# Kernel tuning notes

Measured on AMD Instinct MI355X. Metric: run time of the kernel, lower is better.

Reference implementation:

```python
import jax, jax.numpy as jnp
import numpy as np

N = 100000      # nodes
E = 1200000     # edges
D_IN = 128      # input_dim
H = 64          # hidden_dim
OUT = 3         # output_dim
EPS = 1e-5      # BatchNorm eps


def setup_inputs() -> dict:
    key = jax.random.key(0)
    ks = jax.random.split(key, 24)
    w = lambda k, shape: jax.random.normal(k, shape, jnp.float32) * 0.05
    return {
        "x": jax.random.normal(ks[0], (N, D_IN), jnp.float32),
        "edge_index": jax.random.randint(ks[1], (2, E), 0, N, dtype=jnp.int32),
        "proj_W": w(ks[2], (H, D_IN)), "proj_b": w(ks[3], (H,)),
        "conv1_W": w(ks[4], (H, H)), "conv1_b": w(ks[5], (H,)),
        "bn1_g": jnp.ones((H,), jnp.float32), "bn1_b": w(ks[6], (H,)),
        "conv2_W": w(ks[7], (H, H)), "conv2_b": w(ks[8], (H,)),
        "bn2_g": jnp.ones((H,), jnp.float32), "bn2_b": w(ks[9], (H,)),
        "conv3_W": w(ks[10], (H, H)), "conv3_b": w(ks[11], (H,)),
        "bn3_g": jnp.ones((H,), jnp.float32), "bn3_b": w(ks[12], (H,)),
        "byp_W": w(ks[13], (OUT, D_IN)), "byp_b": w(ks[14], (OUT,)),
        "head_W": w(ks[15], (OUT, H + OUT)), "head_b": w(ks[16], (OUT,)),
    }


def reference(x, edge_index, proj_W, proj_b,
              conv1_W, conv1_b, bn1_g, bn1_b,
              conv2_W, conv2_b, bn2_g, bn2_b,
              conv3_W, conv3_b, bn3_g, bn3_b,
              byp_W, byp_b, head_W, head_b):
    n = x.shape[0]
    row, col = edge_index[0], edge_index[1]
    loop = jnp.arange(n, dtype=row.dtype)
    row_f = jnp.concatenate([row, loop])   # source (with self loops)
    col_f = jnp.concatenate([col, loop])   # target
    # symmetric GCN normalization: deg over targets of A+I, edge weight 1
    deg = jax.ops.segment_sum(jnp.ones(row_f.shape, jnp.float32), col_f, num_segments=n)
    dinv = jnp.where(deg > 0, jax.lax.rsqrt(deg), 0.0)
    norm = dinv[row_f] * dinv[col_f]       # [E+N]

    def gcn(h, W, b):
        h = h @ W.T                                    # transform then propagate
        msg = h[row_f] * norm[:, None]                 # gather + scale
        return jax.ops.segment_sum(msg, col_f, num_segments=n) + b

    def bn(h, g, b):
        # eval-mode BatchNorm1d: running_mean=0, running_var=1 buffers
        return h * (g / jnp.sqrt(1.0 + EPS)) + b

    h = x @ proj_W.T + proj_b
    idn = h
    h = jax.nn.relu(bn(gcn(h, conv1_W, conv1_b), bn1_g, bn1_b)) + idn  # dropout inactive (eval)
    idn = h
    h = jax.nn.relu(bn(gcn(h, conv2_W, conv2_b), bn2_g, bn2_b)) + idn
    h = jax.nn.relu(bn(gcn(h, conv3_W, conv3_b), bn3_g, bn3_b))

    byp = x @ byp_W.T + byp_b
    p = jnp.concatenate([h, byp], axis=1) @ head_W.T + head_b
    kappa = jnp.clip(p[:, 0] * 5.0 + 2.5, 0.2, 10.0)
    alpha = p[:, 1]
    tau = jnp.clip(p[:, 2] + 0.5, 0.05, 2.0)
    return jnp.stack([kappa, alpha, tau], axis=1)
```

## Files before the change

kernel.cpp:

```cpp
#include <hip/hip_runtime.h>
#include <hip/hip_fp16.h>

#define NN 100000
#define NE 1200000
#define NBUK ((NN + 127) / 128)
#define NCHUNK 128

typedef _Float16 h8 __attribute__((ext_vector_type(8)));
typedef float f32x4 __attribute__((ext_vector_type(4)));

__global__ __launch_bounds__(1024) void k_zerob(int* bcnt) {
    int i = threadIdx.x;
    if (i <= NBUK) bcnt[i] = 0;
}

__global__ __launch_bounds__(256) void k_bhist(const int* __restrict__ col, int* __restrict__ bcnt) {
    __shared__ int lh[NBUK];
    for (int i = threadIdx.x; i < NBUK; i += 256) lh[i] = 0;
    __syncthreads();
    for (int e = blockIdx.x * 256 + threadIdx.x; e < NE; e += 256 * 256)
        atomicAdd(&lh[col[e] >> 7], 1);
    __syncthreads();
    for (int i = threadIdx.x; i < NBUK; i += 256) {
        int v = lh[i];
        if (v) atomicAdd(&bcnt[i], v);
    }
}

__global__ __launch_bounds__(1024) void k_bscan(int* __restrict__ bcnt, int* __restrict__ bcur) {
    __shared__ int s[1024];
    int tid = threadIdx.x;
    int v = (tid < NBUK) ? bcnt[tid] : 0;
    s[tid] = v;
    __syncthreads();
    #pragma unroll
    for (int d = 1; d < 1024; d <<= 1) {
        int t = (tid >= d) ? s[tid - d] : 0;
        __syncthreads();
        s[tid] += t;
        __syncthreads();
    }
    if (tid < NBUK) {
        int excl = s[tid] - v;
        bcnt[tid] = excl;
        bcur[tid] = excl;
    }
    if (tid == 0) bcnt[NBUK] = NE;
}

__global__ __launch_bounds__(256) void k_bucket(const int* __restrict__ row,
                                                const int* __restrict__ col,
                                                int* __restrict__ bcur,
                                                unsigned* __restrict__ tmp) {
    __shared__ int lh[NBUK];
    const int tid = threadIdx.x;
    const int per = (NE + NCHUNK - 1) / NCHUNK;
    const int e0 = blockIdx.x * per;
    const int e1 = (e0 + per < NE) ? (e0 + per) : NE;
    for (int i = tid; i < NBUK; i += 256) lh[i] = 0;
    __syncthreads();
    for (int e = e0 + tid; e < e1; e += 256)
        atomicAdd(&lh[col[e] >> 7], 1);
    __syncthreads();
    for (int b = tid; b < NBUK; b += 256) {
        int c = lh[b];
        if (c) lh[b] = atomicAdd(&bcur[b], c);
    }
    __syncthreads();
    for (int e = e0 + tid; e < e1; e += 256) {
        int c = col[e], r = row[e];
        int pos = atomicAdd(&lh[c >> 7], 1);
        tmp[pos] = ((unsigned)r << 7) | (unsigned)(c & 127);
    }
}

__global__ __launch_bounds__(256) void k_build(const unsigned* __restrict__ tmp,
                                               const int* __restrict__ bbase,
                                               int* __restrict__ off,
                                               float* __restrict__ dinv,
                                               int* __restrict__ csr_row) {
    __shared__ int cnt[128], s[128], cur[128];
    const int b = blockIdx.x, tid = threadIdx.x;
    const int colBase = b << 7;
    const int nCols = (NN - colBase < 128) ? (NN - colBase) : 128;
    const int seg0 = bbase[b], seg1 = bbase[b + 1];
    if (tid < 128) cnt[tid] = 0;
    __syncthreads();
    for (int i = seg0 + tid; i < seg1; i += 256)
        atomicAdd(&cnt[tmp[i] & 127], 1);
    __syncthreads();
    if (tid < 128) s[tid] = cnt[tid];
    __syncthreads();
    #pragma unroll
    for (int d = 1; d < 128; d <<= 1) {
        int t = (tid < 128 && tid >= d) ? s[tid - d] : 0;
        __syncthreads();
        if (tid < 128) s[tid] += t;
        __syncthreads();
    }
    if (tid < nCols) {
        int exc = seg0 + s[tid] - cnt[tid];
        off[colBase + tid] = exc;
        cur[tid] = exc;
        dinv[colBase + tid] = rsqrtf((float)cnt[tid] + 1.0f);
    }
    if (b == 0 && tid == 0) off[NN] = NE;
    __syncthreads();
    for (int i = seg0 + tid; i < seg1; i += 256) {
        unsigned v = tmp[i];
        int pos = atomicAdd(&cur[v & 127u], 1);
        csr_row[pos] = (int)(v >> 7);
    }
}

__global__ __launch_bounds__(256) void k_gemmP(const float* __restrict__ X,
                                               const float* __restrict__ W,
                                               const float* __restrict__ bias,
                                               _Float16* __restrict__ Yh,
                                               const float* __restrict__ bypW,
                                               const float* __restrict__ bypb,
                                               float* __restrict__ bypOut,
                                               int n_nodes) {
    constexpr int D = 128, RS = D + 8, KS = D / 32;
    __shared__ _Float16 Xh[64 * RS];
    __shared__ _Float16 Wh[64 * RS];
    const int tid = threadIdx.x;
    const int n0 = blockIdx.x * 64;

    for (int i = tid; i < 64 * (D / 8); i += 256) {
        int j = i / (D / 8), d8 = (i % (D / 8)) * 8;
        const float4* wp = (const float4*)&W[j * D + d8];
        float4 w0 = wp[0], w1 = wp[1];
        h8 h = { (_Float16)w0.x, (_Float16)w0.y, (_Float16)w0.z, (_Float16)w0.w,
                 (_Float16)w1.x, (_Float16)w1.y, (_Float16)w1.z, (_Float16)w1.w };
        *(h8*)&Wh[j * RS + d8] = h;
    }
    for (int i = tid; i < 64 * (D / 8); i += 256) {
        int nl = i / (D / 8), d8 = (i % (D / 8)) * 8;
        int n = n0 + nl; if (n >= n_nodes) n = n_nodes - 1;
        const float4* xp = (const float4*)&X[(size_t)n * D + d8];
        float4 x0 = xp[0], x1 = xp[1];
        h8 h = { (_Float16)x0.x, (_Float16)x0.y, (_Float16)x0.z, (_Float16)x0.w,
                 (_Float16)x1.x, (_Float16)x1.y, (_Float16)x1.z, (_Float16)x1.w };
        *(h8*)&Xh[nl * RS + d8] = h;
    }
    __syncthreads();

    const int wid = tid >> 6, lane = tid & 63;
    const int lm = lane & 15, lq = lane >> 4;
    const int mBase = wid * 16;

    h8 bfrag[4][KS];
    #pragma unroll
    for (int t = 0; t < 4; ++t)
        #pragma unroll
        for (int s = 0; s < KS; ++s)
            bfrag[t][s] = *(const h8*)&Wh[(t * 16 + lm) * RS + s * 32 + lq * 8];

    h8 bfragB[KS];
    #pragma unroll
    for (int s = 0; s < KS; ++s) {
        if (lm < 3) {
            const float4* wp = (const float4*)&bypW[lm * D + s * 32 + lq * 8];
            float4 w0 = wp[0], w1 = wp[1];
            bfragB[s] = (h8){ (_Float16)w0.x, (_Float16)w0.y, (_Float16)w0.z, (_Float16)w0.w,
                              (_Float16)w1.x, (_Float16)w1.y, (_Float16)w1.z, (_Float16)w1.w };
        } else {
            bfragB[s] = (h8)(_Float16)0;
        }
    }

    f32x4 acc[5] = {};
    #pragma unroll
    for (int s = 0; s < KS; ++s) {
        h8 a = *(const h8*)&Xh[(mBase + lm) * RS + s * 32 + lq * 8];
        #pragma unroll
        for (int t = 0; t < 4; ++t)
            acc[t] = __builtin_amdgcn_mfma_f32_16x16x32_f16(a, bfrag[t][s], acc[t], 0, 0, 0);
        acc[4] = __builtin_amdgcn_mfma_f32_16x16x32_f16(a, bfragB[s], acc[4], 0, 0, 0);
    }

    float bb[4];
    #pragma unroll
    for (int t = 0; t < 4; ++t) bb[t] = bias[t * 16 + lm];
    float bypbv = (lm < 3) ? bypb[lm] : 0.f;
    const int nodeBase = n0 + mBase + lq * 4;
    #pragma unroll
    for (int r = 0; r < 4; ++r) {
        int node = nodeBase + r;
        if (node < n_nodes) {
            #pragma unroll
            for (int t = 0; t < 4; ++t)
                Yh[(size_t)node * 64 + t * 16 + lm] = (_Float16)(acc[t][r] + bb[t]);
            if (lm < 3)
                bypOut[node * 3 + lm] = acc[4][r] + bypbv;
        }
    }
}

__global__ __launch_bounds__(256) void k_gemmC(const _Float16* __restrict__ Xhg,
                                               const float* __restrict__ W,
                                               const float* __restrict__ dinv,
                                               _Float16* __restrict__ Yh,
                                               int n_nodes) {
    constexpr int D = 64, RS = D + 8, KS = D / 32;
    __shared__ _Float16 Xh[64 * RS];
    __shared__ _Float16 Wh[64 * RS];
    const int tid = threadIdx.x;
    const int n0 = blockIdx.x * 64;

    for (int i = tid; i < 64 * (D / 8); i += 256) {
        int j = i / (D / 8), d8 = (i % (D / 8)) * 8;
        const float4* wp = (const float4*)&W[j * D + d8];
        float4 w0 = wp[0], w1 = wp[1];
        h8 h = { (_Float16)w0.x, (_Float16)w0.y, (_Float16)w0.z, (_Float16)w0.w,
                 (_Float16)w1.x, (_Float16)w1.y, (_Float16)w1.z, (_Float16)w1.w };
        *(h8*)&Wh[j * RS + d8] = h;
    }
    for (int i = tid; i < 64 * (D / 8); i += 256) {
        int nl = i / (D / 8), d8 = (i % (D / 8)) * 8;
        int n = n0 + nl; if (n >= n_nodes) n = n_nodes - 1;
        *(h8*)&Xh[nl * RS + d8] = *(const h8*)&Xhg[(size_t)n * D + d8];
    }
    __syncthreads();

    const int wid = tid >> 6, lane = tid & 63;
    const int lm = lane & 15, lq = lane >> 4;
    const int mBase = wid * 16;

    h8 bfrag[4][KS];
    #pragma unroll
    for (int t = 0; t < 4; ++t)
        #pragma unroll
        for (int s = 0; s < KS; ++s)
            bfrag[t][s] = *(const h8*)&Wh[(t * 16 + lm) * RS + s * 32 + lq * 8];

    f32x4 acc[4] = {};
    #pragma unroll
    for (int s = 0; s < KS; ++s) {
        h8 a = *(const h8*)&Xh[(mBase + lm) * RS + s * 32 + lq * 8];
        #pragma unroll
        for (int t = 0; t < 4; ++t)
            acc[t] = __builtin_amdgcn_mfma_f32_16x16x32_f16(a, bfrag[t][s], acc[t], 0, 0, 0);
    }

    const int nodeBase = n0 + mBase + lq * 4;
    #pragma unroll
    for (int r = 0; r < 4; ++r) {
        int node = nodeBase + r;
        if (node < n_nodes) {
            float sdv = dinv[node];
            #pragma unroll
            for (int t = 0; t < 4; ++t)
                Yh[(size_t)node * 64 + t * 16 + lm] = (_Float16)(acc[t][r] * sdv);
        }
    }
}

template<bool RES, bool HEAD>
__global__ __launch_bounds__(256) void k_gather(const _Float16* __restrict__ hBh,
                                                const float* __restrict__ dinv,
                                                const int* __restrict__ off,
                                                const int* __restrict__ csr_row,
                                                const float* __restrict__ convb,
                                                const float* __restrict__ bng,
                                                const float* __restrict__ bnb,
                                                _Float16* __restrict__ hA,
                                                const float* __restrict__ byp,
                                                const float* __restrict__ headW,
                                                const float* __restrict__ headb,
                                                float* __restrict__ out) {
    __shared__ float HWs[HEAD ? 204 : 1];
    const int tid = threadIdx.x;
    if constexpr (HEAD) {
        for (int i = tid; i < 204; i += 256)
            HWs[i] = (i < 201) ? headW[i] : headb[i - 201];
        __syncthreads();
    }
    const int wid = tid >> 6, lane = tid & 63;
    const int n = blockIdx.x * 32 + wid * 8 + (lane >> 3);
    const int oct = lane & 7;
    const int f0 = oct * 8;

    const int e0 = off[n], eEnd = off[n + 1];
    const int deg = eEnd - e0;
    int m = deg;
    #pragma unroll
    for (int mask = 8; mask < 64; mask <<= 1) {
        int o = __shfl_xor(m, mask, 64);
        m = (o > m) ? o : m;
    }

    h8 acch = *(const h8*)(hBh + ((size_t)n << 6) + f0);
    const h8 zero = (h8)(_Float16)0;
    for (int it = 0; it < m; it += 2) {
        bool v0 = it < deg, v1 = it + 1 < deg;
        int i0 = e0 + it, i1 = i0 + 1;
        int r0 = csr_row[v0 ? i0 : 0];
        int r1 = csr_row[v1 ? i1 : 0];
        h8 raw0 = *(const h8*)(hBh + ((size_t)r0 << 6) + f0);
        h8 raw1 = *(const h8*)(hBh + ((size_t)r1 << 6) + f0);
        acch = acch + (v0 ? raw0 : zero);
        acch = acch + (v1 ? raw1 : zero);
    }

    const float dv = dinv[n];
    const float bnscale = rsqrtf(1.0f + 1e-5f);
    const float4 cb0 = *(const float4*)&convb[f0], cb1 = *(const float4*)&convb[f0 + 4];
    const float4 g0  = *(const float4*)&bng[f0],  g1  = *(const float4*)&bng[f0 + 4];
    const float4 b0_ = *(const float4*)&bnb[f0],  b1_ = *(const float4*)&bnb[f0 + 4];
    const float cb[8] = { cb0.x, cb0.y, cb0.z, cb0.w, cb1.x, cb1.y, cb1.z, cb1.w };
    const float gg[8] = { g0.x, g0.y, g0.z, g0.w, g1.x, g1.y, g1.z, g1.w };
    const float bb[8] = { b0_.x, b0_.y, b0_.z, b0_.w, b1_.x, b1_.y, b1_.z, b1_.w };
    float v[8];
    #pragma unroll
    for (int j = 0; j < 8; ++j)
        v[j] = fmaxf(((float)acch[j] * dv + cb[j]) * (gg[j] * bnscale) + bb[j], 0.0f);

    if constexpr (!HEAD) {
        size_t o = ((size_t)n << 6) + f0;
        if constexpr (RES) {
            h8 old = *(const h8*)&hA[o];
            #pragma unroll
            for (int j = 0; j < 8; ++j) v[j] += (float)old[j];
        }
        h8 res = { (_Float16)v[0], (_Float16)v[1], (_Float16)v[2], (_Float16)v[3],
                   (_Float16)v[4], (_Float16)v[5], (_Float16)v[6], (_Float16)v[7] };
        *(h8*)&hA[o] = res;
    } else {
        float p[3];
        #pragma unroll
        for (int o = 0; o < 3; ++o) {
            float t = 0.f;
            #pragma unroll
            for (int j = 0; j < 8; ++j) t += v[j] * HWs[o * 67 + f0 + j];
            p[o] = t;
        }
        #pragma unroll
        for (int mask = 1; mask < 8; mask <<= 1) {
            #pragma unroll
            for (int o = 0; o < 3; ++o) p[o] += __shfl_xor(p[o], mask, 64);
        }
        if (oct == 0) {
            float by0 = byp[n * 3], by1 = byp[n * 3 + 1], by2 = byp[n * 3 + 2];
            #pragma unroll
            for (int o = 0; o < 3; ++o)
                p[o] += by0 * HWs[o * 67 + 64] + by1 * HWs[o * 67 + 65] + by2 * HWs[o * 67 + 66]
                      + HWs[201 + o];
            float kappa = fminf(fmaxf(p[0] * 5.0f + 2.5f, 0.2f), 10.0f);
            float tau   = fminf(fmaxf(p[2] + 0.5f, 0.05f), 2.0f);
            out[(size_t)n * 3]     = kappa;
            out[(size_t)n * 3 + 1] = p[1];
            out[(size_t)n * 3 + 2] = tau;
        }
    }
}

extern "C" void kernel_launch(void* const* d_in, const int* in_sizes, int n_in,
                              void* d_out, int out_size, void* d_ws, size_t ws_size,
                              hipStream_t stream) {
    const float* x     = (const float*)d_in[0];
    const int*   ei    = (const int*)d_in[1];
    const int*   row   = ei;
    const int*   col   = ei + NE;
    const float* projW = (const float*)d_in[2];
    const float* projb = (const float*)d_in[3];
    const float* convW[3] = { (const float*)d_in[4], (const float*)d_in[8],  (const float*)d_in[12] };
    const float* convb[3] = { (const float*)d_in[5], (const float*)d_in[9],  (const float*)d_in[13] };
    const float* bng[3]   = { (const float*)d_in[6], (const float*)d_in[10], (const float*)d_in[14] };
    const float* bnb[3]   = { (const float*)d_in[7], (const float*)d_in[11], (const float*)d_in[15] };
    const float* bypW  = (const float*)d_in[16];
    const float* bypb  = (const float*)d_in[17];
    const float* headW = (const float*)d_in[18];
    const float* headb = (const float*)d_in[19];
    float* out = (float*)d_out;

    float*    ws   = (float*)d_ws;
    float*    dinv = ws;
    _Float16* hAh  = (_Float16*)(ws + 102400);
    _Float16* hBh  = hAh + (size_t)NN * 64;
    float*    byp  = (float*)(hBh + (size_t)NN * 64);
    int*      off     = (int*)(byp + 300032);
    int*      csr_row = off + 100096;
    int*      bcnt    = csr_row + NE;
    int*      bcur    = bcnt + 784;
    unsigned* tmp     = (unsigned*)hAh;

    k_zerob<<<1, 1024, 0, stream>>>(bcnt);
    k_bhist<<<256, 256, 0, stream>>>(col, bcnt);
    k_bscan<<<1, 1024, 0, stream>>>(bcnt, bcur);
    k_bucket<<<NCHUNK, 256, 0, stream>>>(row, col, bcur, tmp);
    k_build<<<NBUK, 256, 0, stream>>>(tmp, bcnt, off, dinv, csr_row);

    k_gemmP<<<(NN + 63) / 64, 256, 0, stream>>>(x, projW, projb, hAh, bypW, bypb, byp, NN);

    for (int l = 0; l < 3; l++) {
        k_gemmC<<<(NN + 63) / 64, 256, 0, stream>>>(hAh, convW[l], dinv, hBh, NN);
        if (l < 2)
            k_gather<true, false><<<NN / 32, 256, 0, stream>>>(
                hBh, dinv, off, csr_row, convb[l], bng[l], bnb[l], hAh,
                nullptr, nullptr, nullptr, nullptr);
        else
            k_gather<false, true><<<NN / 32, 256, 0, stream>>>(
                hBh, dinv, off, csr_row, convb[l], bng[l], bnb[l], nullptr,
                byp, headW, headb, out);
    }
}
```

Baseline: 293.3 us.

## Sort nodes by in-degree so gather wavefronts process similar-degree nodes

Adds a counting sort of nodes by in-degree (clamped at 63), built from a histogram, a scan and a scatter kernel, and has the gather kernels process nodes in that permuted order. Each wavefront handles 8 nodes and loops to the maximum degree among them, so grouping similar degrees is meant to cut idle lanes from load imbalance. The cost is three extra small kernel launches and an extra indirection per node, and nodes within a wavefront are no longer adjacent, so their feature-row loads and writes become scattered.

```diff
diff --git a/kernel.cpp b/kernel.cpp
--- a/kernel.cpp
+++ b/kernel.cpp
@@ -9,9 +9,10 @@
 typedef _Float16 h8 __attribute__((ext_vector_type(8)));
 typedef float f32x4 __attribute__((ext_vector_type(4)));
 
-__global__ __launch_bounds__(1024) void k_zerob(int* bcnt) {
+__global__ __launch_bounds__(1024) void k_zerob(int* bcnt, int* degcnt) {
     int i = threadIdx.x;
     if (i <= NBUK) bcnt[i] = 0;
+    if (i < 64) degcnt[i] = 0;
 }
 
 __global__ __launch_bounds__(256) void k_bhist(const int* __restrict__ col, int* __restrict__ bcnt) {
@@ -110,6 +111,64 @@
         unsigned v = tmp[i];
         int pos = atomicAdd(&cur[v & 127u], 1);
         csr_row[pos] = (int)(v >> 7);
+    }
+}
+
+__global__ __launch_bounds__(256) void k_deghist(const int* __restrict__ off, int* __restrict__ degcnt) {
+    __shared__ int dh[64];
+    int tid = threadIdx.x;
+    if (tid < 64) dh[tid] = 0;
+    __syncthreads();
+    int i = blockIdx.x * 256 + tid;
+    if (i < NN) {
+        int d = off[i + 1] - off[i]; if (d > 63) d = 63;
+        atomicAdd(&dh[d], 1);
+    }
+    __syncthreads();
+    if (tid < 64) {
+        int v = dh[tid];
+        if (v) atomicAdd(&degcnt[tid], v);
+    }
+}
+
+__global__ __launch_bounds__(64) void k_degscan(int* __restrict__ degcnt, int* __restrict__ degcur) {
+    __shared__ int s[64];
+    int tid = threadIdx.x;
+    int v = degcnt[tid];
+    s[tid] = v;
+    __syncthreads();
+    #pragma unroll
+    for (int d = 1; d < 64; d <<= 1) {
+        int t = (tid >= d) ? s[tid - d] : 0;
+        __syncthreads();
+        s[tid] += t;
+        __syncthreads();
+    }
+    degcur[tid] = s[tid] - v;
+}
+
+__global__ __launch_bounds__(256) void k_perm(const int* __restrict__ off,
+                                              int* __restrict__ degcur,
+                                              int* __restrict__ perm) {
+    __shared__ int dh[64];
+    int tid = threadIdx.x;
+    if (tid < 64) dh[tid] = 0;
+    __syncthreads();
+    int i = blockIdx.x * 256 + tid;
+    int d = -1;
+    if (i < NN) {
+        d = off[i + 1] - off[i]; if (d > 63) d = 63;
+        atomicAdd(&dh[d], 1);
+    }
+    __syncthreads();
+    if (tid < 64) {
+        int c = dh[tid];
+        if (c) dh[tid] = atomicAdd(&degcur[tid], c);
+    }
+    __syncthreads();
+    if (i < NN) {
+        int pos = atomicAdd(&dh[d], 1);
+        perm[pos] = i;
     }
 }
 
@@ -262,6 +321,7 @@
                                                 const float* __restrict__ dinv,
                                                 const int* __restrict__ off,
                                                 const int* __restrict__ csr_row,
+                                                const int* __restrict__ perm,
                                                 const float* __restrict__ convb,
                                                 const float* __restrict__ bng,
                                                 const float* __restrict__ bnb,
@@ -278,7 +338,8 @@
         __syncthreads();
     }
     const int wid = tid >> 6, lane = tid & 63;
-    const int n = blockIdx.x * 32 + wid * 8 + (lane >> 3);
+    const int slot = blockIdx.x * 32 + wid * 8 + (lane >> 3);
+    const int n = perm[slot];
     const int oct = lane & 7;
     const int f0 = oct * 8;
 
@@ -384,25 +445,32 @@
     int*      csr_row = off + 100096;
     int*      bcnt    = csr_row + NE;
     int*      bcur    = bcnt + 784;
+    int*      perm    = bcur + 784;
+    int*      degcnt  = perm + 100096;
+    int*      degcur  = degcnt + 64;
     unsigned* tmp     = (unsigned*)hAh;
 
-    k_zerob<<<1, 1024, 0, stream>>>(bcnt);
+    k_zerob<<<1, 1024, 0, stream>>>(bcnt, degcnt);
     k_bhist<<<256, 256, 0, stream>>>(col, bcnt);
     k_bscan<<<1, 1024, 0, stream>>>(bcnt, bcur);
     k_bucket<<<NCHUNK, 256, 0, stream>>>(row, col, bcur, tmp);
     k_build<<<NBUK, 256, 0, stream>>>(tmp, bcnt, off, dinv, csr_row);
 
+    k_deghist<<<(NN + 255) / 256, 256, 0, stream>>>(off, degcnt);
+    k_degscan<<<1, 64, 0, stream>>>(degcnt, degcur);
+    k_perm<<<(NN + 255) / 256, 256, 0, stream>>>(off, degcur, perm);
+
     k_gemmP<<<(NN + 63) / 64, 256, 0, stream>>>(x, projW, projb, hAh, bypW, bypb, byp, NN);
 
     for (int l = 0; l < 3; l++) {
         k_gemmC<<<(NN + 63) / 64, 256, 0, stream>>>(hAh, convW[l], dinv, hBh, NN);
         if (l < 2)
             k_gather<true, false><<<NN / 32, 256, 0, stream>>>(
-                hBh, dinv, off, csr_row, convb[l], bng[l], bnb[l], hAh,
+                hBh, dinv, off, csr_row, perm, convb[l], bng[l], bnb[l], hAh,
                 nullptr, nullptr, nullptr, nullptr);
         else
             k_gather<false, true><<<NN / 32, 256, 0, stream>>>(
-                hBh, dinv, off, csr_row, convb[l], bng[l], bnb[l], nullptr,
+                hBh, dinv, off, csr_row, perm, convb[l], bng[l], bnb[l], nullptr,
                 byp, headW, headb, out);
     }
 }
```

Measured after the change: 315.3 us. 7.5% more time.

## Sort nodes by degree within windows to balance gather wavefront work

Applied to the files above, without the earlier changes.

Adds a kernel that counting-sorts nodes by in-degree inside each 1024-node window and writes a permutation. The gather kernels then take node ids through this permutation, so the 8 nodes sharing a wavefront have similar degrees and less time is lost to the max-degree loop bound. The cost is one extra small kernel, an extra indirection per node, and less locality in the output writes and self-feature reads.

```diff
diff --git a/kernel.cpp b/kernel.cpp
--- a/kernel.cpp
+++ b/kernel.cpp
@@ -5,6 +5,8 @@
 #define NE 1200000
 #define NBUK ((NN + 127) / 128)
 #define NCHUNK 128
+#define WSZ 1024
+#define NWIN ((NN + WSZ - 1) / WSZ)
 
 typedef _Float16 h8 __attribute__((ext_vector_type(8)));
 typedef float f32x4 __attribute__((ext_vector_type(4)));
@@ -110,6 +112,38 @@
         unsigned v = tmp[i];
         int pos = atomicAdd(&cur[v & 127u], 1);
         csr_row[pos] = (int)(v >> 7);
+    }
+}
+
+__global__ __launch_bounds__(256) void k_wsort(const int* __restrict__ off, int* __restrict__ perm) {
+    __shared__ int cnt[64], cur[64];
+    const int tid = threadIdx.x;
+    const int wbase = blockIdx.x * WSZ;
+    const int nNodes = (NN - wbase < WSZ) ? (NN - wbase) : WSZ;
+    if (tid < 64) cnt[tid] = 0;
+    __syncthreads();
+    for (int i = tid; i < nNodes; i += 256) {
+        int n = wbase + i;
+        int d = off[n + 1] - off[n]; if (d > 63) d = 63;
+        atomicAdd(&cnt[d], 1);
+    }
+    __syncthreads();
+    if (tid < 64) cur[tid] = cnt[tid];
+    __syncthreads();
+    #pragma unroll
+    for (int d = 1; d < 64; d <<= 1) {
+        int t = (tid < 64 && tid >= d) ? cur[tid - d] : 0;
+        __syncthreads();
+        if (tid < 64) cur[tid] += t;
+        __syncthreads();
+    }
+    if (tid < 64) cur[tid] -= cnt[tid];
+    __syncthreads();
+    for (int i = tid; i < nNodes; i += 256) {
+        int n = wbase + i;
+        int d = off[n + 1] - off[n]; if (d > 63) d = 63;
+        int pos = atomicAdd(&cur[d], 1);
+        perm[wbase + pos] = n;
     }
 }
 
@@ -262,6 +296,7 @@
                                                 const float* __restrict__ dinv,
                                                 const int* __restrict__ off,
                                                 const int* __restrict__ csr_row,
+                                                const int* __restrict__ perm,
                                                 const float* __restrict__ convb,
                                                 const float* __restrict__ bng,
                                                 const float* __restrict__ bnb,
@@ -278,7 +313,8 @@
         __syncthreads();
     }
     const int wid = tid >> 6, lane = tid & 63;
-    const int n = blockIdx.x * 32 + wid * 8 + (lane >> 3);
+    const int slot = blockIdx.x * 32 + wid * 8 + (lane >> 3);
+    const int n = perm[slot];
     const int oct = lane & 7;
     const int f0 = oct * 8;
 
@@ -384,6 +420,7 @@
     int*      csr_row = off + 100096;
     int*      bcnt    = csr_row + NE;
     int*      bcur    = bcnt + 784;
+    int*      perm    = bcur + 784;
     unsigned* tmp     = (unsigned*)hAh;
 
     k_zerob<<<1, 1024, 0, stream>>>(bcnt);
@@ -392,17 +429,19 @@
     k_bucket<<<NCHUNK, 256, 0, stream>>>(row, col, bcur, tmp);
     k_build<<<NBUK, 256, 0, stream>>>(tmp, bcnt, off, dinv, csr_row);
 
+    k_wsort<<<NWIN, 256, 0, stream>>>(off, perm);
+
     k_gemmP<<<(NN + 63) / 64, 256, 0, stream>>>(x, projW, projb, hAh, bypW, bypb, byp, NN);
 
     for (int l = 0; l < 3; l++) {
         k_gemmC<<<(NN + 63) / 64, 256, 0, stream>>>(hAh, convW[l], dinv, hBh, NN);
         if (l < 2)
             k_gather<true, false><<<NN / 32, 256, 0, stream>>>(
-                hBh, dinv, off, csr_row, convb[l], bng[l], bnb[l], hAh,
+                hBh, dinv, off, csr_row, perm, convb[l], bng[l], bnb[l], hAh,
                 nullptr, nullptr, nullptr, nullptr);
         else
             k_gather<false, true><<<NN / 32, 256, 0, stream>>>(
-                hBh, dinv, off, csr_row, convb[l], bng[l], bnb[l], nullptr,
+                hBh, dinv, off, csr_row, perm, convb[l], bng[l], bnb[l], nullptr,
                 byp, headW, headb, out);
     }
 }
```

Measured after the change: 314.8 us. +7.3%, slower.
